# Kernel tuning notes

Hardware: AMD Instinct MI355X
Metric: run time of the kernel (lower is better)

## Reference

```python
import jax, jax.numpy as jnp
import numpy as np
import math

# Static config derived from init_kwargs
B, L, D, H, NL = 256, 256, 128, 2, 2
E = D // H                       # 64
F = L // 2 + 1                   # 129 rfft bins
SR = 0.6                         # sample_ratio (> 1/n_layers)
STEP = (F * (1.0 - SR)) // (NL - 1)          # 51.0, python float floor-div as in torch code
LEFTS = [int(F * (1.0 - SR) - k * STEP) for k in range(NL)]   # [51, 0]
RIGHTS = [int(F - k * STEP) for k in range(NL)]               # [129, 78]
TOPK = max(int(1 * math.log(L)), 1)          # factor=1 -> 5
NUM_TOTAL = 100000                           # user_num + item_num
SPATIAL_RATIO = 0.1
INV_SQRT_E = 1.0 / math.sqrt(E)
INV_SQRT_2 = 1.0 / math.sqrt(2.0)


def setup_inputs() -> dict:
    key = jax.random.key(0)
    ks = jax.random.split(key, 12)
    s = 0.05
    return {
        "paths": jax.random.randint(ks[0], (B, L), 0, NUM_TOTAL),
        "lengths": jax.random.randint(ks[1], (B,), 1, L + 1),
        "degrees": jax.random.randint(ks[2], (B,), 0, 64),
        "training": 1,
        "ego_emb": jax.random.normal(ks[3], (NUM_TOTAL + 1, D), jnp.float32) * s,
        "pos_emb": jax.random.normal(ks[4], (L, D), jnp.float32) * s,
        "Wq": jax.random.normal(ks[5], (NL, D, D), jnp.float32) * s,
        "Wk": jax.random.normal(ks[6], (NL, D, D), jnp.float32) * s,
        "Wv": jax.random.normal(ks[7], (NL, D, D), jnp.float32) * s,
        "Wp": jax.random.normal(ks[8], (NL, D, D), jnp.float32) * s,
        "F1": jax.random.normal(ks[9], (NL, D, 2 * D), jnp.float32) * s,
        "F2": jax.random.normal(ks[10], (NL, 2 * D, D), jnp.float32) * s,
    }


def _hybrid_attention(k, x, mask, Wq, Wk, Wv, Wp):
    # project and split heads: [B,H,E,L]
    def proj(W):
        return (x @ W).reshape(B, L, H, E).transpose(0, 2, 3, 1)
    q, kk, v = proj(Wq), proj(Wk), proj(Wv)
    qf = jnp.fft.rfft(q, axis=-1)   # [B,H,E,F] complex
    kf = jnp.fft.rfft(kk, axis=-1)
    vf = jnp.fft.rfft(v, axis=-1)
    l, r = LEFTS[k], RIGHTS[k]
    # frequency-band attention: band-limited cross-correlation (scatter back == zero-pad)
    res = qf[..., l:r] * jnp.conj(kf[..., l:r])
    box = jnp.zeros(qf.shape, dtype=res.dtype).at[..., l:r].set(res)
    corr = jnp.fft.irfft(box, n=L, axis=-1)          # [B,H,E,L]
    mean_value = jnp.mean(corr, axis=(1, 2))         # [B,L]
    # training branch: global topk delays (shared across batch), roll-based aggregation
    _, delays = jax.lax.top_k(jnp.mean(mean_value, axis=0), TOPK)   # [TOPK]
    weights = mean_value[:, delays]                  # [B,TOPK]
    tmp_corr = jax.nn.softmax(weights, axis=-1)      # [B,TOPK]
    # roll(v, -d) along time == gather at (t + d) % L
    idx = (jnp.arange(L)[None, :] + delays[:, None]) % L            # [TOPK,L]
    gathered = v[:, :, :, idx]                       # [B,H,E,TOPK,L]
    freq = jnp.einsum('bhetl,bt->bhel', gathered, tmp_corr)
    freq = freq.transpose(0, 3, 1, 2).reshape(B, L, D)
    # dual-domain: time attention on band-limited signals (std=True -> same band)
    def band_ifft(f):
        padded = jnp.zeros(f.shape, dtype=f.dtype).at[..., l:r].set(f[..., l:r])
        return jnp.fft.irfft(padded, n=L, axis=-1).transpose(0, 1, 3, 2)   # [B,H,L,E]
    qt, kt, vt = band_ifft(qf), band_ifft(kf), band_ifft(vf)
    scores = jnp.einsum('bhqe,bhke->bhqk', qt, kt) * INV_SQRT_E + mask
    att = jax.nn.softmax(scores, axis=-1)
    spatial = jnp.einsum('bhqk,bhke->bhqe', att, vt).transpose(0, 2, 1, 3).reshape(B, L, D)
    out = (1.0 - SPATIAL_RATIO) * freq + SPATIAL_RATIO * spatial
    return out @ Wp + x


def reference(paths, lengths, degrees, training, ego_emb, pos_emb, Wq, Wk, Wv, Wp, F1, F2):
    del degrees, training  # degrees unused; training branch baked in (training=True)
    x = ego_emb[paths] + pos_emb[None, :, :]         # [B,L,D]
    m = (paths < NUM_TOTAL).astype(jnp.float32)
    mask = ((1.0 - m) * -10000.0)[:, None, None, :]  # [B,1,1,L]
    for k in range(NL):
        a = _hybrid_attention(k, x, mask, Wq[k], Wk[k], Wv[k], Wp[k])
        h = a @ F1[k]
        h = h * 0.5 * (1.0 + jax.lax.erf(h * INV_SQRT_2))   # exact GELU
        x = h @ F2[k]
    # gather last valid position per sequence
    return x[jnp.arange(B), lengths - 1]             # [B,D]
```

## Files before the change

kernel.cpp:

```cpp
#include <hip/hip_runtime.h>
#include <math.h>

#define Bn 256
#define Ln 256
#define Dn 128
#define Hn 2
#define En 64
#define NLn 2
#define TOPKn 5
#define NUM_TOTALn 100000
#define BLD (Bn*Ln*Dn)
#define WT_LAYER 147456

using frag_ab = __attribute__((ext_vector_type(8))) short;
using frag_cd = __attribute__((ext_vector_type(4))) float;

__device__ inline short f2bf(float f) {
    union { float f; unsigned u; } c; c.f = f;
    unsigned r = (c.u + 0x7FFFu + ((c.u >> 16) & 1u)) >> 16;
    return (short)r;
}
__device__ inline float bf2f(short s) {
    union { unsigned u; float f; } c; c.u = ((unsigned)(unsigned short)s) << 16;
    return c.f;
}

__global__ void beacon_kernel(float* out, float v) { out[0] = v; }

__global__ __launch_bounds__(256) void build_G_kernel(short* __restrict__ G) {
    int k = blockIdx.x, t = blockIdx.y, s = threadIdx.x;
    int d = (t - s) & 255;
    int f1 = (k == 0) ? 51 : 1;
    int f2 = (k == 0) ? 127 : 77;
    float acc;
    if (d == 0) {
        acc = 2.0f * (float)(f2 - f1 + 1);
    } else {
        const float c = 3.14159265358979323846f / 256.0f;
        int ahi = (d * (2 * f2 + 1)) & 511;
        int alo = (d * (2 * f1 - 1)) & 511;
        acc = (sinf(c * (float)ahi) - sinf(c * (float)alo)) / sinf(c * (float)d);
    }
    acc += (k == 0) ? ((d & 1) ? -1.0f : 1.0f)
                    : 1.0f;
    G[((size_t)k * 256 + t) * 256 + s] = f2bf(acc * (1.0f / 256.0f));
}

__global__ __launch_bounds__(256) void build_x_kernel(const int* __restrict__ paths,
                                                      const float* __restrict__ ego,
                                                      const float* __restrict__ pos,
                                                      short* __restrict__ x) {
    int base = (blockIdx.x * 256 + threadIdx.x) * 4;
    int d = base & 127;
    int bl = base >> 7;
    int t = bl & 255;
    float4 e = *(const float4*)(ego + (size_t)paths[bl] * Dn + d);
    float4 p = *(const float4*)(pos + t * Dn + d);
    short4 s;
    s.x = f2bf(e.x + p.x); s.y = f2bf(e.y + p.y);
    s.z = f2bf(e.z + p.z); s.w = f2bf(e.w + p.w);
    *(short4*)&x[base] = s;
}

__global__ __launch_bounds__(256) void wtrans_all_kernel(
        const float* __restrict__ Wq, const float* __restrict__ Wk,
        const float* __restrict__ Wv, const float* __restrict__ Wp,
        const float* __restrict__ F1, const float* __restrict__ F2,
        short* __restrict__ Wt) {
    int z = blockIdx.y;
    int idx = blockIdx.x * 256 + threadIdx.x;
    short* WtL = Wt + (size_t)z * WT_LAYER;
    if (idx < 65536) {
        int which = idx >> 14, local = idx & 16383;
        const float* src = (which == 0) ? Wq : (which == 1) ? Wk
                         : (which == 2) ? Wv : Wp;
        float scale = (which == 3) ? 0.1f : 1.0f;
        int n = local & 127, k = local >> 7;
        WtL[(which << 14) + n * 128 + k] = f2bf(scale * src[(size_t)z * 16384 + local]);
    } else if (idx < 98304) {
        int local = idx - 65536;
        int n = local & 255, k = local >> 8;
        WtL[65536 + n * 128 + k] = f2bf(F1[(size_t)z * 32768 + local]);
    } else {
        int local = idx - 98304;
        int n = local & 127, k = local >> 7;
        WtL[98304 + n * 256 + k] = f2bf(F2[(size_t)z * 32768 + local]);
    }
}

template<bool BT_FAST, bool GELU_EPI>
__global__ __launch_bounds__(256)
void mfma_gemm_kernel(const short* A, const short* Bp, short* C, const short* R,
                      int K, int lda, int ldb, int ldc, int ldr,
                      long long sA, long long sB, long long sC, long long sR,
                      long long sCsplit, float alpha, float beta) {
    int bz = blockIdx.z;
    A += (size_t)bz * sA; C += (size_t)bz * sC;
    if (R) R += (size_t)bz * sR;
    const short* Bt = Bp + (size_t)bz * sB;
    const int m0 = blockIdx.x * 128, n0 = blockIdx.y * 128;
    int n0c = n0;
    if (sCsplit) { C += (size_t)blockIdx.y * sCsplit; n0c = 0; }
    __shared__ short As[128 * 40];
    __shared__ short Bs[128 * 40];
    int tid = threadIdx.x;
    int lane = tid & 63, wave = tid >> 6;
    int wr = (wave >> 1) * 64, wc = (wave & 1) * 64;
    int l15 = lane & 15, qd = lane >> 4;

    frag_cd zero4 = {0.f, 0.f, 0.f, 0.f};
    frag_cd acc[4][4];
    #pragma unroll
    for (int i = 0; i < 4; i++)
        #pragma unroll
        for (int j = 0; j < 4; j++) acc[i][j] = zero4;

    int arow = tid >> 1, acg = (tid & 1) * 16;
    int bnrow = tid >> 1, bcg = (tid & 1) * 16;
    int bkk = tid & 31, bnb = (tid >> 5) * 16;

    int4 pa0, pa1, pb0, pb1;
    {
        const short* ap = A + (size_t)(m0 + arow) * lda + acg;
        pa0 = *(const int4*)ap; pa1 = *(const int4*)(ap + 8);
        if (BT_FAST) {
            const short* bp = Bt + (size_t)(n0 + bnrow) * ldb + bcg;
            pb0 = *(const int4*)bp; pb1 = *(const int4*)(bp + 8);
        } else {
            const short* bp = Bt + (size_t)bkk * ldb + n0 + bnb;
            pb0 = *(const int4*)bp; pb1 = *(const int4*)(bp + 8);
        }
    }

    for (int k0 = 0; k0 < K; k0 += 32) {
        __syncthreads();
        *(int4*)&As[arow * 40 + acg] = pa0;
        *(int4*)&As[arow * 40 + acg + 8] = pa1;
        if (BT_FAST) {
            *(int4*)&Bs[bnrow * 40 + bcg] = pb0;
            *(int4*)&Bs[bnrow * 40 + bcg + 8] = pb1;
        } else {
            short tmp[16];
            *(int4*)&tmp[0] = pb0; *(int4*)&tmp[8] = pb1;
            #pragma unroll
            for (int i = 0; i < 16; i++) Bs[(bnb + i) * 40 + bkk] = tmp[i];
        }
        __syncthreads();
        if (k0 + 32 < K) {
            const short* ap = A + (size_t)(m0 + arow) * lda + k0 + 32 + acg;
            pa0 = *(const int4*)ap; pa1 = *(const int4*)(ap + 8);
            if (BT_FAST) {
                const short* bp = Bt + (size_t)(n0 + bnrow) * ldb + k0 + 32 + bcg;
                pb0 = *(const int4*)bp; pb1 = *(const int4*)(bp + 8);
            } else {
                const short* bp = Bt + (size_t)(k0 + 32 + bkk) * ldb + n0 + bnb;
                pb0 = *(const int4*)bp; pb1 = *(const int4*)(bp + 8);
            }
        }
        frag_ab af[4], bf[4];
        #pragma unroll
        for (int ms = 0; ms < 4; ms++)
            af[ms] = *(frag_ab*)&As[(wr + ms * 16 + l15) * 40 + qd * 8];
        #pragma unroll
        for (int ns = 0; ns < 4; ns++)
            bf[ns] = *(frag_ab*)&Bs[(wc + ns * 16 + l15) * 40 + qd * 8];
        #pragma unroll
        for (int ms = 0; ms < 4; ms++)
            #pragma unroll
            for (int ns = 0; ns < 4; ns++)
                acc[ms][ns] = __builtin_amdgcn_mfma_f32_16x16x32_bf16(
                    bf[ns], af[ms], acc[ms][ns], 0, 0, 0);
    }
    #pragma unroll
    for (int ms = 0; ms < 4; ms++) {
        int m = m0 + wr + ms * 16 + l15;
        #pragma unroll
        for (int ns = 0; ns < 4; ns++) {
            int nb = wc + ns * 16 + qd * 4;
            float v[4];
            #pragma unroll
            for (int r = 0; r < 4; r++) v[r] = alpha * acc[ms][ns][r];
            if (R) {
                short4 r4 = *(const short4*)&R[(size_t)m * ldr + n0 + nb];
                v[0] += beta * bf2f(r4.x); v[1] += beta * bf2f(r4.y);
                v[2] += beta * bf2f(r4.z); v[3] += beta * bf2f(r4.w);
            }
            if (GELU_EPI) {
                #pragma unroll
                for (int r = 0; r < 4; r++)
                    v[r] = v[r] * 0.5f * (1.0f + erff(v[r] * 0.70710678118654752f));
            }
            short4 o;
            o.x = f2bf(v[0]); o.y = f2bf(v[1]); o.z = f2bf(v[2]); o.w = f2bf(v[3]);
            *(short4*)&C[(size_t)m * ldc + n0c + nb] = o;
        }
    }
}

static inline void mgemm(hipStream_t s, const short* A, const short* B, short* C,
                         const short* R, int M, int N, int K,
                         int lda, int ldb, int ldc, int ldr,
                         long long sA, long long sB, long long sC, long long sR,
                         int batch, float alpha, float beta, bool btFast, bool gelu,
                         long long sCsplit = 0) {
    dim3 grid(M / 128, N / 128, batch), block(256);
    if (btFast) {
        if (gelu) mfma_gemm_kernel<true, true ><<<grid, block, 0, s>>>(A, B, C, R, K, lda, ldb, ldc, ldr, sA, sB, sC, sR, sCsplit, alpha, beta);
        else      mfma_gemm_kernel<true, false><<<grid, block, 0, s>>>(A, B, C, R, K, lda, ldb, ldc, ldr, sA, sB, sC, sR, sCsplit, alpha, beta);
    } else {
        if (gelu) mfma_gemm_kernel<false, true ><<<grid, block, 0, s>>>(A, B, C, R, K, lda, ldb, ldc, ldr, sA, sB, sC, sR, sCsplit, alpha, beta);
        else      mfma_gemm_kernel<false, false><<<grid, block, 0, s>>>(A, B, C, R, K, lda, ldb, ldc, ldr, sA, sB, sC, sR, sCsplit, alpha, beta);
    }
}

__global__ __launch_bounds__(512)
void filtproj_kernel(const short* __restrict__ G, const short* __restrict__ x,
                     const short* __restrict__ W, short* __restrict__ q) {
    int b = blockIdx.x;
    __shared__ short As[256 * 40];
    __shared__ short Bs[128 * 40];
    __shared__ short xf[256 * 136];
    int tid = threadIdx.x;
    int lane = tid & 63, wave = tid >> 6;
    int wr = (wave & 3) * 64, wc = (wave >> 2) * 64;
    int l15 = lane & 15, qd = lane >> 4;
    const short* xb = x + ((size_t)b << 15);

    frag_cd zero4 = {0.f, 0.f, 0.f, 0.f};
    frag_cd acc[4][4];
    #pragma unroll
    for (int i = 0; i < 4; i++)
        #pragma unroll
        for (int j = 0; j < 4; j++) acc[i][j] = zero4;

    int arow = tid >> 1, acg = (tid & 1) * 16;
    int bkk = tid & 31, bnb = (tid >> 5) * 16;

    int4 pa0, pa1, pb0, pb1;
    {
        const short* ap = G + (size_t)arow * 256 + acg;
        pa0 = *(const int4*)ap; pa1 = *(const int4*)(ap + 8);
        if (tid < 256) {
            const short* bp = xb + (size_t)bkk * 128 + bnb;
            pb0 = *(const int4*)bp; pb1 = *(const int4*)(bp + 8);
        }
    }
    for (int k0 = 0; k0 < 256; k0 += 32) {
        __syncthreads();
        *(int4*)&As[arow * 40 + acg] = pa0;
        *(int4*)&As[arow * 40 + acg + 8] = pa1;
        if (tid < 256) {
            short tmp[16];
            *(int4*)&tmp[0] = pb0; *(int4*)&tmp[8] = pb1;
            #pragma unroll
            for (int i = 0; i < 16; i++) Bs[(bnb + i) * 40 + bkk] = tmp[i];
        }
        __syncthreads();
        if (k0 + 32 < 256) {
            const short* ap = G + (size_t)arow * 256 + k0 + 32 + acg;
            pa0 = *(const int4*)ap; pa1 = *(const int4*)(ap + 8);
            if (tid < 256) {
                const short* bp = xb + (size_t)(k0 + 32 + bkk) * 128 + bnb;
                pb0 = *(const int4*)bp; pb1 = *(const int4*)(bp + 8);
            }
        }
        frag_ab af[4], bf[4];
        #pragma unroll
        for (int ms = 0; ms < 4; ms++)
            af[ms] = *(frag_ab*)&As[(wr + ms * 16 + l15) * 40 + qd * 8];
        #pragma unroll
        for (int ns = 0; ns < 4; ns++)
            bf[ns] = *(frag_ab*)&Bs[(wc + ns * 16 + l15) * 40 + qd * 8];
        #pragma unroll
        for (int ms = 0; ms < 4; ms++)
            #pragma unroll
            for (int ns = 0; ns < 4; ns++)
                acc[ms][ns] = __builtin_amdgcn_mfma_f32_16x16x32_bf16(
                    bf[ns], af[ms], acc[ms][ns], 0, 0, 0);
    }
    #pragma unroll
    for (int ms = 0; ms < 4; ms++) {
        int m = wr + ms * 16 + l15;
        #pragma unroll
        for (int ns = 0; ns < 4; ns++) {
            int nb = wc + ns * 16 + qd * 4;
            short4 o;
            o.x = f2bf(acc[ms][ns][0]); o.y = f2bf(acc[ms][ns][1]);
            o.z = f2bf(acc[ms][ns][2]); o.w = f2bf(acc[ms][ns][3]);
            *(short4*)&xf[m * 136 + nb] = o;
        }
    }

    int brow = tid >> 2, bcg = (tid & 3) * 8;
    #pragma unroll 1
    for (int y = 0; y < 3; y++) {
        const short* Bt = W + y * 16384;
        #pragma unroll
        for (int i = 0; i < 4; i++)
            #pragma unroll
            for (int j = 0; j < 4; j++) acc[i][j] = zero4;
        int4 pb = *(const int4*)(Bt + (size_t)brow * 128 + bcg);
        for (int k0 = 0; k0 < 128; k0 += 32) {
            __syncthreads();
            *(int4*)&Bs[brow * 40 + bcg] = pb;
            __syncthreads();
            if (k0 + 32 < 128)
                pb = *(const int4*)(Bt + (size_t)brow * 128 + k0 + 32 + bcg);
            frag_ab af[4], bf[4];
            #pragma unroll
            for (int ms = 0; ms < 4; ms++)
                af[ms] = *(frag_ab*)&xf[(wr + ms * 16 + l15) * 136 + k0 + qd * 8];
            #pragma unroll
            for (int ns = 0; ns < 4; ns++)
                bf[ns] = *(frag_ab*)&Bs[(wc + ns * 16 + l15) * 40 + qd * 8];
            #pragma unroll
            for (int ms = 0; ms < 4; ms++)
                #pragma unroll
                for (int ns = 0; ns < 4; ns++)
                    acc[ms][ns] = __builtin_amdgcn_mfma_f32_16x16x32_bf16(
                        bf[ns], af[ms], acc[ms][ns], 0, 0, 0);
        }
        short* Cy = q + (size_t)y * BLD + ((size_t)b << 15);
        #pragma unroll
        for (int ms = 0; ms < 4; ms++) {
            int m = wr + ms * 16 + l15;
            #pragma unroll
            for (int ns = 0; ns < 4; ns++) {
                int nb = wc + ns * 16 + qd * 4;
                short4 o;
                o.x = f2bf(acc[ms][ns][0]); o.y = f2bf(acc[ms][ns][1]);
                o.z = f2bf(acc[ms][ns][2]); o.w = f2bf(acc[ms][ns][3]);
                *(short4*)&Cy[(size_t)m * 128 + nb] = o;
            }
        }
    }
}

__global__ __launch_bounds__(512)
void amix_ffn_kernel(const short* __restrict__ x, const short* __restrict__ q,
                     const short* __restrict__ W,
                     const float* __restrict__ tc, const int* __restrict__ delays,
                     short* __restrict__ xout) {
    int b = blockIdx.x;
    __shared__ short aL[256 * 132];
    __shared__ short hA[256 * 132];
    int tid = threadIdx.x;
    int lane = tid & 63, wave = tid >> 6;
    int wr = (wave & 3) * 64, wc = (wave >> 2) * 64;
    int l15 = lane & 15, qd = lane >> 4;
    const short* xb = x + ((size_t)b << 15);

    float wj[TOPKn]; int dj[TOPKn];
    #pragma unroll
    for (int j = 0; j < TOPKn; j++) {
        wj[j] = tc[b * TOPKn + j];
        dj[j] = delays[j];
    }

    frag_cd zero4 = {0.f, 0.f, 0.f, 0.f};

    {
        int arow = tid >> 1, acg = (tid & 1) * 16;
        #pragma unroll
        for (int k0 = 0; k0 < 128; k0 += 32) {
            #pragma unroll
            for (int c = 0; c < 2; c++) {
                int col = k0 + acg + c * 8;
                float m8[8] = {0.f, 0.f, 0.f, 0.f, 0.f, 0.f, 0.f, 0.f};
                #pragma unroll
                for (int j = 0; j < TOPKn; j++) {
                    frag_ab v = *(const frag_ab*)(xb + (((arow + dj[j]) & 255) << 7) + col);
                    #pragma unroll
                    for (int i = 0; i < 8; i++) m8[i] += wj[j] * bf2f(v[i]);
                }
                frag_ab o;
                #pragma unroll
                for (int i = 0; i < 8; i++) o[i] = f2bf(m8[i]);
                *(frag_ab*)&hA[arow * 132 + col] = o;
            }
        }
        const short* qb = q + ((size_t)b << 15);
        #pragma unroll
        for (int p = 0; p < 8; p++) {
            int chunk = p * 512 + tid;
            int r = chunk >> 4, cb = (chunk & 15) * 8;
            *(frag_ab*)&aL[r * 132 + cb] = *(const frag_ab*)(qb + (size_t)r * 128 + cb);
        }
    }
    __syncthreads();

    frag_cd acc[4][4];
    #pragma unroll
    for (int i = 0; i < 4; i++)
        #pragma unroll
        for (int j = 0; j < 4; j++) acc[i][j] = zero4;
    {
        const short* Bt = W + 131072;
        for (int k0 = 0; k0 < 128; k0 += 32) {
            frag_ab af[4], bf[4];
            #pragma unroll
            for (int ms = 0; ms < 4; ms++)
                af[ms] = *(frag_ab*)&hA[(wr + ms * 16 + l15) * 132 + k0 + qd * 8];
            #pragma unroll
            for (int ns = 0; ns < 4; ns++)
                bf[ns] = *(const frag_ab*)(Bt + (size_t)(wc + ns * 16 + l15) * 128 + k0 + qd * 8);
            #pragma unroll
            for (int ms = 0; ms < 4; ms++)
                #pragma unroll
                for (int ns = 0; ns < 4; ns++)
                    acc[ms][ns] = __builtin_amdgcn_mfma_f32_16x16x32_bf16(
                        bf[ns], af[ms], acc[ms][ns], 0, 0, 0);
        }
    }
    {
        const short* Bt = W + 49152;
        for (int k0 = 0; k0 < 128; k0 += 32) {
            frag_ab af[4], bf[4];
            #pragma unroll
            for (int ms = 0; ms < 4; ms++)
                af[ms] = *(frag_ab*)&aL[(wr + ms * 16 + l15) * 132 + k0 + qd * 8];
            #pragma unroll
            for (int ns = 0; ns < 4; ns++)
                bf[ns] = *(const frag_ab*)(Bt + (size_t)(wc + ns * 16 + l15) * 128 + k0 + qd * 8);
            #pragma unroll
            for (int ms = 0; ms < 4; ms++)
                #pragma unroll
                for (int ns = 0; ns < 4; ns++)
                    acc[ms][ns] = __builtin_amdgcn_mfma_f32_16x16x32_bf16(
                        bf[ns], af[ms], acc[ms][ns], 0, 0, 0);
        }
    }
    __syncthreads();
    #pragma unroll
    for (int ms = 0; ms < 4; ms++) {
        int m = wr + ms * 16 + l15;
        #pragma unroll
        for (int ns = 0; ns < 4; ns++) {
            int nb = wc + ns * 16 + qd * 4;
            short4 r4 = *(const short4*)&xb[(size_t)m * 128 + nb];
            float v[4];
            v[0] = acc[ms][ns][0] + bf2f(r4.x);
            v[1] = acc[ms][ns][1] + bf2f(r4.y);
            v[2] = acc[ms][ns][2] + bf2f(r4.z);
            v[3] = acc[ms][ns][3] + bf2f(r4.w);
            short4 o;
            o.x = f2bf(v[0]); o.y = f2bf(v[1]); o.z = f2bf(v[2]); o.w = f2bf(v[3]);
            *(short4*)&aL[m * 132 + nb] = o;
        }
    }
    __syncthreads();

    const short* F1T = W + 65536;
    const short* F2T = W + 98304;
    frag_cd xacc[4][4];
    #pragma unroll
    for (int i = 0; i < 4; i++)
        #pragma unroll
        for (int j = 0; j < 4; j++) xacc[i][j] = zero4;

    #pragma unroll 1
    for (int half = 0; half < 2; half++) {
        const short* B1 = F1T + (size_t)(half * 128) * 128;
        frag_cd hacc[4][4];
        #pragma unroll
        for (int i = 0; i < 4; i++)
            #pragma unroll
            for (int j = 0; j < 4; j++) hacc[i][j] = zero4;
        for (int k0 = 0; k0 < 128; k0 += 32) {
            frag_ab af[4], bf[4];
            #pragma unroll
            for (int ms = 0; ms < 4; ms++)
                af[ms] = *(frag_ab*)&aL[(wr + ms * 16 + l15) * 132 + k0 + qd * 8];
            #pragma unroll
            for (int ns = 0; ns < 4; ns++)
                bf[ns] = *(const frag_ab*)(B1 + (size_t)(wc + ns * 16 + l15) * 128 + k0 + qd * 8);
            #pragma unroll
            for (int ms = 0; ms < 4; ms++)
                #pragma unroll
                for (int ns = 0; ns < 4; ns++)
                    hacc[ms][ns] = __builtin_amdgcn_mfma_f32_16x16x32_bf16(
                        bf[ns], af[ms], hacc[ms][ns], 0, 0, 0);
        }
        __syncthreads();
        #pragma unroll
        for (int ms = 0; ms < 4; ms++) {
            int m = wr + ms * 16 + l15;
            #pragma unroll
            for (int ns = 0; ns < 4; ns++) {
                int nb = wc + ns * 16 + qd * 4;
                float v[4];
                #pragma unroll
                for (int r = 0; r < 4; r++) {
                    float t = hacc[ms][ns][r];
                    v[r] = t * 0.5f * (1.0f + erff(t * 0.70710678118654752f));
                }
                short4 o;
                o.x = f2bf(v[0]); o.y = f2bf(v[1]);
                o.z = f2bf(v[2]); o.w = f2bf(v[3]);
                *(short4*)&hA[m * 132 + nb] = o;
            }
        }
        __syncthreads();

        for (int k0 = 0; k0 < 128; k0 += 32) {
            frag_ab af[4], bf[4];
            #pragma unroll
            for (int ms = 0; ms < 4; ms++)
                af[ms] = *(frag_ab*)&hA[(wr + ms * 16 + l15) * 132 + k0 + qd * 8];
            #pragma unroll
            for (int ns = 0; ns < 4; ns++)
                bf[ns] = *(const frag_ab*)(F2T + (size_t)(wc + ns * 16 + l15) * 256 + half * 128 + k0 + qd * 8);
            #pragma unroll
            for (int ms = 0; ms < 4; ms++)
                #pragma unroll
                for (int ns = 0; ns < 4; ns++)
                    xacc[ms][ns] = __builtin_amdgcn_mfma_f32_16x16x32_bf16(
                        bf[ns], af[ms], xacc[ms][ns], 0, 0, 0);
        }
    }
    short* xo = xout + ((size_t)b << 15);
    #pragma unroll
    for (int ms = 0; ms < 4; ms++) {
        int m = wr + ms * 16 + l15;
        #pragma unroll
        for (int ns = 0; ns < 4; ns++) {
            int nb = wc + ns * 16 + qd * 4;
            short4 o;
            o.x = f2bf(xacc[ms][ns][0]); o.y = f2bf(xacc[ms][ns][1]);
            o.z = f2bf(xacc[ms][ns][2]); o.w = f2bf(xacc[ms][ns][3]);
            *(short4*)&xo[(size_t)m * 128 + nb] = o;
        }
    }
}

__global__ __launch_bounds__(512, 4) void attn_kernel(short* q,
        const short* __restrict__ kb, const short* __restrict__ vf,
        const int* __restrict__ paths, float* __restrict__ mv2) {
    int h = blockIdx.x, b = blockIdx.y;
    __shared__ short SB[256 * 72];
    __shared__ short ks[64 * 72];
    __shared__ short vT[80 * 72];
    __shared__ float masks[256];
    __shared__ float mvpart[512];
    int tid = threadIdx.x;
    int lane = tid & 63, wave = tid >> 6;
    int l15 = lane & 15, qd = lane >> 4;
    if (tid < 256) masks[tid] = (paths[b * 256 + tid] < NUM_TOTALn) ? 0.0f : -10000.0f;
    {
        int e0 = tid * 2;
        #pragma unroll
        for (int i = 0; i < 2; i++) {
            int e = e0 + i;
            int row = 64 + (e >> 6), col = e & 63;
            vT[row * 72 + col] = (row == 64) ? (short)0x3F80 : (short)0;
        }
    }
    short* qg = q + ((size_t)b << 15) + (size_t)h * 64;
    const short* kg = kb + ((size_t)b << 15) + (size_t)h * 64;
    const short* vg = vf + ((size_t)b << 15) + (size_t)h * 64;

    #pragma unroll
    for (int p = 0; p < 4; p++) {
        int chunk = p * 512 + tid;
        int r = chunk >> 3, cb = (chunk & 7) * 8;
        *(frag_ab*)&SB[r * 72 + cb] = *(const frag_ab*)(qg + (size_t)r * 128 + cb);
    }
    __syncthreads();
    int myrow = wave * 32;
    frag_ab aq[2][2];
    #pragma unroll
    for (int mt = 0; mt < 2; mt++)
        #pragma unroll
        for (int hf = 0; hf < 2; hf++)
            aq[mt][hf] = *(frag_ab*)&SB[(myrow + mt * 16 + l15) * 72 + hf * 32 + qd * 8];

    frag_cd zero4 = {0.f, 0.f, 0.f, 0.f};
    frag_cd oacc[2][5];
    #pragma unroll
    for (int mt = 0; mt < 2; mt++)
        #pragma unroll
        for (int et = 0; et < 5; et++) oacc[mt][et] = zero4;
    float macc = 0.0f;
    int tau = tid & 255, half = tid >> 8;

    for (int jt = 0; jt < 4; jt++) {
        __syncthreads();
        {
            int r = tid >> 3, cb = (tid & 7) * 8;
            *(frag_ab*)&ks[r * 72 + cb] =
                *(const frag_ab*)(kg + (size_t)(jt * 64 + r) * 128 + cb);
            frag_ab v8 = *(const frag_ab*)(vg + (size_t)(jt * 64 + r) * 128 + cb);
            int swz = (((r >> 3) ^ (cb >> 3)) << 3) + (r & 7);
            #pragma unroll
            for (int i = 0; i < 8; i++) vT[(cb + i) * 72 + swz] = v8[i];
        }
        __syncthreads();
        #pragma unroll
        for (int mt = 0; mt < 2; mt++) {
            #pragma unroll
            for (int nt = 0; nt < 4; nt++) {
                frag_ab b0 = *(frag_ab*)&ks[(nt * 16 + l15) * 72 + qd * 8];
                frag_ab b1 = *(frag_ab*)&ks[(nt * 16 + l15) * 72 + 32 + qd * 8];
                frag_cd c = zero4;
                c = __builtin_amdgcn_mfma_f32_16x16x32_bf16(aq[mt][0], b0, c, 0, 0, 0);
                c = __builtin_amdgcn_mfma_f32_16x16x32_bf16(aq[mt][1], b1, c, 0, 0, 0);
                int keyLocal = nt * 16 + l15;
                #pragma unroll
                for (int r = 0; r < 4; r++) {
                    int row = myrow + mt * 16 + qd * 4 + r;
                    int tt = (row - jt * 64 - keyLocal) & 255;
                    SB[tt * 66 + keyLocal] = f2bf(c[r] * 0.125f);
                }
            }
        }
        __syncthreads();
        {
            const int* SD32 = (const int*)&SB[tau * 66 + half * 32];
            #pragma unroll
            for (int i = 0; i < 16; i++) {
                int pk = SD32[i];
                macc += bf2f((short)(pk & 0xFFFF)) + bf2f((short)(pk >> 16));
            }
        }
        #pragma unroll
        for (int mt = 0; mt < 2; mt++) {
            int row = myrow + mt * 16 + l15;
            #pragma unroll
            for (int hf = 0; hf < 2; hf++) {
                int kl0 = hf * 32 + qd * 8;
                frag_ab pfrag;
                #pragma unroll
                for (int j = 0; j < 8; j++) {
                    int kl = kl0 + j;
                    int tt = (row - jt * 64 - kl) & 255;
                    float s = bf2f(SB[tt * 66 + kl]);
                    pfrag[j] = f2bf(__expf(s + masks[jt * 64 + kl]));
                }
                #pragma unroll
                for (int et = 0; et < 5; et++) {
                    int e = et * 16 + l15;
                    int blk = (hf * 4 + qd) ^ ((e >> 3) & 7);
                    frag_ab bv = *(frag_ab*)&vT[e * 72 + (blk << 3)];
                    oacc[mt][et] = __builtin_amdgcn_mfma_f32_16x16x32_bf16(pfrag, bv, oacc[mt][et], 0, 0, 0);
                }
            }
        }
    }
    __syncthreads();
    mvpart[tid] = macc;
    __syncthreads();
    if (tid < 256)
        mv2[(size_t)h * 65536 + b * 256 + tid] =
            (mvpart[tid] + mvpart[tid + 256]) * 0.0625f;
    #pragma unroll
    for (int mt = 0; mt < 2; mt++) {
        #pragma unroll
        for (int r = 0; r < 4; r++) {
            float l = oacc[mt][4][r];
            l = __shfl(l, (lane & 48));
            float inv = 1.0f / l;
            int row = myrow + mt * 16 + qd * 4 + r;
            #pragma unroll
            for (int et = 0; et < 4; et++)
                qg[(size_t)row * 128 + et * 16 + l15] = f2bf(oacc[mt][et][r] * inv);
        }
    }
}

__global__ __launch_bounds__(256) void gm_reduce_kernel(const float* __restrict__ mv2,
                                                        float* __restrict__ gm) {
    int tau = blockIdx.x;
    int b = threadIdx.x;
    __shared__ float red[256];
    red[b] = mv2[b * 256 + tau] + mv2[65536 + b * 256 + tau];
    __syncthreads();
    for (int s = 128; s > 0; s >>= 1) { if (b < s) red[b] += red[b + s]; __syncthreads(); }
    if (b == 0) gm[tau] = red[0] * (1.0f / 256.0f);
}

__global__ __launch_bounds__(256) void topk_softmax_kernel(const float* __restrict__ gm,
                                                           const float* __restrict__ mv2,
                                                           int* __restrict__ delays,
                                                           float* __restrict__ tc) {
    __shared__ float vsh[4];
    __shared__ int ish[4];
    __shared__ int dsh[TOPKn];
    int tid = threadIdx.x;
    int lane = tid & 63, wave = tid >> 6;
    float v = gm[tid];
    for (int t = 0; t < TOPKn; t++) {
        float mv_ = v; int mi = tid;
        #pragma unroll
        for (int s = 32; s > 0; s >>= 1) {
            float v2 = __shfl_xor(mv_, s); int i2 = __shfl_xor(mi, s);
            if (v2 > mv_ || (v2 == mv_ && i2 < mi)) { mv_ = v2; mi = i2; }
        }
        if (lane == 0) { vsh[wave] = mv_; ish[wave] = mi; }
        __syncthreads();
        if (tid == 0) {
            float bv = vsh[0]; int bi = ish[0];
            #pragma unroll
            for (int w = 1; w < 4; w++)
                if (vsh[w] > bv || (vsh[w] == bv && ish[w] < bi)) { bv = vsh[w]; bi = ish[w]; }
            dsh[t] = bi; delays[t] = bi;
        }
        __syncthreads();
        if (tid == dsh[t]) v = -1e30f;
    }
    __syncthreads();
    int b = tid;
    float w[TOPKn];
    float m = -1e30f;
    #pragma unroll
    for (int j = 0; j < TOPKn; j++) {
        w[j] = mv2[b * 256 + dsh[j]] + mv2[65536 + b * 256 + dsh[j]];
        m = fmaxf(m, w[j]);
    }
    float ssum = 0.0f;
    #pragma unroll
    for (int j = 0; j < TOPKn; j++) { w[j] = expf(w[j] - m); ssum += w[j]; }
    #pragma unroll
    for (int j = 0; j < TOPKn; j++) tc[b * TOPKn + j] = w[j] / ssum;
}

__global__ __launch_bounds__(256) void gather_out_kernel(const short* __restrict__ x,
                                                         const int* __restrict__ lengths,
                                                         float* __restrict__ out) {
    int idx = blockIdx.x * 256 + threadIdx.x;
    int d = idx & 127;
    int b = idx >> 7;
    out[idx] = bf2f(x[((size_t)b << 15) + (size_t)(lengths[b] - 1) * Dn + d]);
}

extern "C" void kernel_launch(void* const* d_in, const int* in_sizes, int n_in,
                              void* d_out, int out_size, void* d_ws, size_t ws_size,
                              hipStream_t stream) {
    const int* paths    = (const int*)d_in[0];
    const int* lengths  = (const int*)d_in[1];
    const float* ego    = (const float*)d_in[4];
    const float* pos    = (const float*)d_in[5];
    const float* Wq     = (const float*)d_in[6];
    const float* Wk     = (const float*)d_in[7];
    const float* Wv     = (const float*)d_in[8];
    const float* Wp     = (const float*)d_in[9];
    const float* F1     = (const float*)d_in[10];
    const float* F2     = (const float*)d_in[11];
    float* out = (float*)d_out;

    const size_t need = (size_t)5 * BLD * 2 + 131072 * 2 + 131072 * 4
                        + 256 * 4 + 1280 * 4 + 16 * 4 + (size_t)NLn * WT_LAYER * 2;
    if (ws_size < need) {
        beacon_kernel<<<dim3(1), dim3(1), 0, stream>>>(out, (float)(ws_size >> 20));
        return;
    }

    short* x    = (short*)d_ws;
    short* q    = x + (size_t)1 * BLD;
    short* kb   = x + (size_t)2 * BLD;
    short* vf   = x + (size_t)3 * BLD;
    short* Gb   = x + (size_t)5 * BLD;
    float* mv   = (float*)(Gb + 131072);
    float* gm   = mv + 131072;
    float* tc   = gm + 256;
    int* delays = (int*)(tc + 1280);
    short* Wt   = (short*)(delays + 16);

    build_G_kernel<<<dim3(2, 256), dim3(256), 0, stream>>>(Gb);
    build_x_kernel<<<dim3(BLD / 1024), dim3(256), 0, stream>>>(paths, ego, pos, x);

    wtrans_all_kernel<<<dim3(512, NLn), dim3(256), 0, stream>>>(Wq, Wk, Wv, Wp, F1, F2, Wt);
    mgemm(stream, Wt + 49152, Wt + 32768, Wt + 131072, nullptr,
          128, 128, 128, 128, 128, 128, 0,
          WT_LAYER, WT_LAYER, WT_LAYER, 0, NLn,
          9.0f, 0.0f, false, false);

    for (int k = 0; k < NLn; k++) {
        const short* WtL = Wt + (size_t)k * WT_LAYER;
        filtproj_kernel<<<dim3(256), dim3(512), 0, stream>>>(
            Gb + (size_t)k * 65536, x, WtL, q);

        attn_kernel<<<dim3(2, 256), dim3(512), 0, stream>>>(q, kb, vf, paths, mv);

        gm_reduce_kernel<<<dim3(256), dim3(256), 0, stream>>>(mv, gm);
        topk_softmax_kernel<<<dim3(1), dim3(256), 0, stream>>>(gm, mv, delays, tc);

        amix_ffn_kernel<<<dim3(256), dim3(512), 0, stream>>>(
            x, q, WtL, tc, delays, x);
    }

    gather_out_kernel<<<dim3((Bn * Dn) / 256), dim3(256), 0, stream>>>(x, lengths, out);
}
```

Before: 364.5 us.

## Split amix_ffn across two row-half blocks and stage weight tiles in LDS

The fused auto-correlation mix plus FFN kernel now launches two 256-thread blocks per batch element, each handling 128 sequence rows. This halves per-block shared memory so more blocks can be resident and gives more blocks overall. Weight fragments for every GEMM stage are now staged through a small LDS tile with a register prefetch of the next k-slice, instead of being read straight from global memory by every wave. The kernel still updates x in place, but a block now reads delay-shifted rows that may belong to the other half while that half's block writes them, which is a cross-block read/write race.

New measurement: 357.9 us. Within noise of the previous version (-1.8%).

```diff
diff --git a/kernel.cpp b/kernel.cpp
--- a/kernel.cpp
+++ b/kernel.cpp
@@ -336,17 +336,19 @@
     }
 }
 
-__global__ __launch_bounds__(512)
+__global__ __launch_bounds__(256)
 void amix_ffn_kernel(const short* __restrict__ x, const short* __restrict__ q,
                      const short* __restrict__ W,
                      const float* __restrict__ tc, const int* __restrict__ delays,
                      short* __restrict__ xout) {
-    int b = blockIdx.x;
-    __shared__ short aL[256 * 132];
-    __shared__ short hA[256 * 132];
+    int half = blockIdx.x, b = blockIdx.y;
+    const int m0 = half * 128;
+    __shared__ short aL[128 * 132];
+    __shared__ short hA[128 * 132];
+    __shared__ short Bs[128 * 40];
     int tid = threadIdx.x;
     int lane = tid & 63, wave = tid >> 6;
-    int wr = (wave & 3) * 64, wc = (wave >> 2) * 64;
+    int wr = (wave >> 1) * 64, wc = (wave & 1) * 64;
     int l15 = lane & 15, qd = lane >> 4;
     const short* xb = x + ((size_t)b << 15);
 
@@ -369,7 +371,7 @@
                 float m8[8] = {0.f, 0.f, 0.f, 0.f, 0.f, 0.f, 0.f, 0.f};
                 #pragma unroll
                 for (int j = 0; j < TOPKn; j++) {
-                    frag_ab v = *(const frag_ab*)(xb + (((arow + dj[j]) & 255) << 7) + col);
+                    frag_ab v = *(const frag_ab*)(xb + (((m0 + arow + dj[j]) & 255) << 7) + col);
                     #pragma unroll
                     for (int i = 0; i < 8; i++) m8[i] += wj[j] * bf2f(v[i]);
                 }
@@ -379,31 +381,45 @@
                 *(frag_ab*)&hA[arow * 132 + col] = o;
             }
         }
-        const short* qb = q + ((size_t)b << 15);
+        const short* qb = q + ((size_t)b << 15) + (size_t)m0 * 128;
         #pragma unroll
         for (int p = 0; p < 8; p++) {
-            int chunk = p * 512 + tid;
+            int chunk = p * 256 + tid;
             int r = chunk >> 4, cb = (chunk & 15) * 8;
             *(frag_ab*)&aL[r * 132 + cb] = *(const frag_ab*)(qb + (size_t)r * 128 + cb);
         }
     }
     __syncthreads();
 
+    int brow = tid >> 1, bcg = (tid & 1) * 16;
+
     frag_cd acc[4][4];
     #pragma unroll
     for (int i = 0; i < 4; i++)
         #pragma unroll
         for (int j = 0; j < 4; j++) acc[i][j] = zero4;
-    {
-        const short* Bt = W + 131072;
+    #pragma unroll 1
+    for (int pass = 0; pass < 2; pass++) {
+        const short* Bt = W + (pass ? 49152 : 131072);
+        const short* Asrc = pass ? aL : hA;
+        int4 pb0 = *(const int4*)(Bt + (size_t)brow * 128 + bcg);
+        int4 pb1 = *(const int4*)(Bt + (size_t)brow * 128 + bcg + 8);
         for (int k0 = 0; k0 < 128; k0 += 32) {
+            __syncthreads();
+            *(int4*)&Bs[brow * 40 + bcg] = pb0;
+            *(int4*)&Bs[brow * 40 + bcg + 8] = pb1;
+            __syncthreads();
+            if (k0 + 32 < 128) {
+                pb0 = *(const int4*)(Bt + (size_t)brow * 128 + k0 + 32 + bcg);
+                pb1 = *(const int4*)(Bt + (size_t)brow * 128 + k0 + 32 + bcg + 8);
+            }
             frag_ab af[4], bf[4];
             #pragma unroll
             for (int ms = 0; ms < 4; ms++)
-                af[ms] = *(frag_ab*)&hA[(wr + ms * 16 + l15) * 132 + k0 + qd * 8];
+                af[ms] = *(frag_ab*)&Asrc[(wr + ms * 16 + l15) * 132 + k0 + qd * 8];
             #pragma unroll
             for (int ns = 0; ns < 4; ns++)
-                bf[ns] = *(const frag_ab*)(Bt + (size_t)(wc + ns * 16 + l15) * 128 + k0 + qd * 8);
+                bf[ns] = *(frag_ab*)&Bs[(wc + ns * 16 + l15) * 40 + qd * 8];
             #pragma unroll
             for (int ms = 0; ms < 4; ms++)
                 #pragma unroll
@@ -412,24 +428,6 @@
                         bf[ns], af[ms], acc[ms][ns], 0, 0, 0);
         }
     }
-    {
-        const short* Bt = W + 49152;
-        for (int k0 = 0; k0 < 128; k0 += 32) {
-            frag_ab af[4], bf[4];
-            #pragma unroll
-            for (int ms = 0; ms < 4; ms++)
-                af[ms] = *(frag_ab*)&aL[(wr + ms * 16 + l15) * 132 + k0 + qd * 8];
-            #pragma unroll
-            for (int ns = 0; ns < 4; ns++)
-                bf[ns] = *(const frag_ab*)(Bt + (size_t)(wc + ns * 16 + l15) * 128 + k0 + qd * 8);
-            #pragma unroll
-            for (int ms = 0; ms < 4; ms++)
-                #pragma unroll
-                for (int ns = 0; ns < 4; ns++)
-                    acc[ms][ns] = __builtin_amdgcn_mfma_f32_16x16x32_bf16(
-                        bf[ns], af[ms], acc[ms][ns], 0, 0, 0);
-        }
-    }
     __syncthreads();
     #pragma unroll
     for (int ms = 0; ms < 4; ms++) {
@@ -437,7 +435,7 @@
         #pragma unroll
         for (int ns = 0; ns < 4; ns++) {
             int nb = wc + ns * 16 + qd * 4;
-            short4 r4 = *(const short4*)&xb[(size_t)m * 128 + nb];
+            short4 r4 = *(const short4*)&xb[(size_t)(m0 + m) * 128 + nb];
             float v[4];
             v[0] = acc[ms][ns][0] + bf2f(r4.x);
             v[1] = acc[ms][ns][1] + bf2f(r4.y);
@@ -459,27 +457,39 @@
         for (int j = 0; j < 4; j++) xacc[i][j] = zero4;
 
     #pragma unroll 1
-    for (int half = 0; half < 2; half++) {
-        const short* B1 = F1T + (size_t)(half * 128) * 128;
+    for (int f1h = 0; f1h < 2; f1h++) {
+        const short* B1 = F1T + (size_t)(f1h * 128) * 128;
         frag_cd hacc[4][4];
         #pragma unroll
         for (int i = 0; i < 4; i++)
             #pragma unroll
             for (int j = 0; j < 4; j++) hacc[i][j] = zero4;
-        for (int k0 = 0; k0 < 128; k0 += 32) {
-            frag_ab af[4], bf[4];
-            #pragma unroll
-            for (int ms = 0; ms < 4; ms++)
-                af[ms] = *(frag_ab*)&aL[(wr + ms * 16 + l15) * 132 + k0 + qd * 8];
-            #pragma unroll
-            for (int ns = 0; ns < 4; ns++)
-                bf[ns] = *(const frag_ab*)(B1 + (size_t)(wc + ns * 16 + l15) * 128 + k0 + qd * 8);
-            #pragma unroll
-            for (int ms = 0; ms < 4; ms++)
+        {
+            int4 pb0 = *(const int4*)(B1 + (size_t)brow * 128 + bcg);
+            int4 pb1 = *(const int4*)(B1 + (size_t)brow * 128 + bcg + 8);
+            for (int k0 = 0; k0 < 128; k0 += 32) {
+                __syncthreads();
+                *(int4*)&Bs[brow * 40 + bcg] = pb0;
+                *(int4*)&Bs[brow * 40 + bcg + 8] = pb1;
+                __syncthreads();
+                if (k0 + 32 < 128) {
+                    pb0 = *(const int4*)(B1 + (size_t)brow * 128 + k0 + 32 + bcg);
+                    pb1 = *(const int4*)(B1 + (size_t)brow * 128 + k0 + 32 + bcg + 8);
+                }
+                frag_ab af[4], bf[4];
+                #pragma unroll
+                for (int ms = 0; ms < 4; ms++)
+                    af[ms] = *(frag_ab*)&aL[(wr + ms * 16 + l15) * 132 + k0 + qd * 8];
                 #pragma unroll
                 for (int ns = 0; ns < 4; ns++)
-                    hacc[ms][ns] = __builtin_amdgcn_mfma_f32_16x16x32_bf16(
-                        bf[ns], af[ms], hacc[ms][ns], 0, 0, 0);
+                    bf[ns] = *(frag_ab*)&Bs[(wc + ns * 16 + l15) * 40 + qd * 8];
+                #pragma unroll
+                for (int ms = 0; ms < 4; ms++)
+                    #pragma unroll
+                    for (int ns = 0; ns < 4; ns++)
+                        hacc[ms][ns] = __builtin_amdgcn_mfma_f32_16x16x32_bf16(
+                            bf[ns], af[ms], hacc[ms][ns], 0, 0, 0);
+            }
         }
         __syncthreads();
         #pragma unroll
@@ -502,23 +512,35 @@
         }
         __syncthreads();
 
-        for (int k0 = 0; k0 < 128; k0 += 32) {
-            frag_ab af[4], bf[4];
-            #pragma unroll
-            for (int ms = 0; ms < 4; ms++)
-                af[ms] = *(frag_ab*)&hA[(wr + ms * 16 + l15) * 132 + k0 + qd * 8];
-            #pragma unroll
-            for (int ns = 0; ns < 4; ns++)
-                bf[ns] = *(const frag_ab*)(F2T + (size_t)(wc + ns * 16 + l15) * 256 + half * 128 + k0 + qd * 8);
-            #pragma unroll
-            for (int ms = 0; ms < 4; ms++)
+        {
+            int4 pb0 = *(const int4*)(F2T + (size_t)brow * 256 + f1h * 128 + bcg);
+            int4 pb1 = *(const int4*)(F2T + (size_t)brow * 256 + f1h * 128 + bcg + 8);
+            for (int k0 = 0; k0 < 128; k0 += 32) {
+                __syncthreads();
+                *(int4*)&Bs[brow * 40 + bcg] = pb0;
+                *(int4*)&Bs[brow * 40 + bcg + 8] = pb1;
+                __syncthreads();
+                if (k0 + 32 < 128) {
+                    pb0 = *(const int4*)(F2T + (size_t)brow * 256 + f1h * 128 + k0 + 32 + bcg);
+                    pb1 = *(const int4*)(F2T + (size_t)brow * 256 + f1h * 128 + k0 + 32 + bcg + 8);
+                }
+                frag_ab af[4], bf[4];
+                #pragma unroll
+                for (int ms = 0; ms < 4; ms++)
+                    af[ms] = *(frag_ab*)&hA[(wr + ms * 16 + l15) * 132 + k0 + qd * 8];
                 #pragma unroll
                 for (int ns = 0; ns < 4; ns++)
-                    xacc[ms][ns] = __builtin_amdgcn_mfma_f32_16x16x32_bf16(
-                        bf[ns], af[ms], xacc[ms][ns], 0, 0, 0);
-        }
-    }
-    short* xo = xout + ((size_t)b << 15);
+                    bf[ns] = *(frag_ab*)&Bs[(wc + ns * 16 + l15) * 40 + qd * 8];
+                #pragma unroll
+                for (int ms = 0; ms < 4; ms++)
+                    #pragma unroll
+                    for (int ns = 0; ns < 4; ns++)
+                        xacc[ms][ns] = __builtin_amdgcn_mfma_f32_16x16x32_bf16(
+                            bf[ns], af[ms], xacc[ms][ns], 0, 0, 0);
+            }
+        }
+    }
+    short* xo = xout + ((size_t)b << 15) + (size_t)m0 * 128;
     #pragma unroll
     for (int ms = 0; ms < 4; ms++) {
         int m = wr + ms * 16 + l15;
@@ -784,7 +806,7 @@
         gm_reduce_kernel<<<dim3(256), dim3(256), 0, stream>>>(mv, gm);
         topk_softmax_kernel<<<dim3(1), dim3(256), 0, stream>>>(gm, mv, delays, tc);
 
-        amix_ffn_kernel<<<dim3(256), dim3(512), 0, stream>>>(
+        amix_ffn_kernel<<<dim3(2, 256), dim3(256), 0, stream>>>(
             x, q, WtL, tc, delays, x);
     }
 
```

## Stage weight tiles through double-buffered shared memory in amix_ffn GEMMs

Applied to the files above, without the earlier changes.

The B-operand (weight) fragments in all four GEMM loops of amix_ffn_kernel were read straight from global memory by every wave, with each weight row fetched by four waves. Now each 128x32 K-slice is loaded cooperatively, one int4 per thread, into a padded, double-buffered LDS tile, with the next slice prefetched into registers. This cuts duplicate global/L2 traffic and makes the loads coalesced. In exchange it adds a __syncthreads per K-step and about 20KB more LDS on top of about 135KB already used, which may be tight or limit occupancy.

Measured after the change: 352.0 us. 1.04x faster.

```diff
diff --git a/kernel.cpp b/kernel.cpp
--- a/kernel.cpp
+++ b/kernel.cpp
@@ -344,6 +344,7 @@
     int b = blockIdx.x;
     __shared__ short aL[256 * 132];
     __shared__ short hA[256 * 132];
+    __shared__ short Bs[2][128 * 40];
     int tid = threadIdx.x;
     int lane = tid & 63, wave = tid >> 6;
     int wr = (wave & 3) * 64, wc = (wave >> 2) * 64;
@@ -389,39 +390,31 @@
     }
     __syncthreads();
 
+    int brow = tid >> 2, bcg = (tid & 3) * 8;
+
     frag_cd acc[4][4];
     #pragma unroll
     for (int i = 0; i < 4; i++)
         #pragma unroll
         for (int j = 0; j < 4; j++) acc[i][j] = zero4;
-    {
-        const short* Bt = W + 131072;
-        for (int k0 = 0; k0 < 128; k0 += 32) {
+    #pragma unroll 1
+    for (int pass = 0; pass < 2; pass++) {
+        const short* Bt = W + (pass ? 49152 : 131072);
+        const short* Asrc = pass ? aL : hA;
+        int4 pb = *(const int4*)(Bt + (size_t)brow * 128 + bcg);
+        int cur = 0;
+        for (int k0 = 0; k0 < 128; k0 += 32, cur ^= 1) {
+            *(int4*)&Bs[cur][brow * 40 + bcg] = pb;
+            if (k0 + 32 < 128)
+                pb = *(const int4*)(Bt + (size_t)brow * 128 + k0 + 32 + bcg);
+            __syncthreads();
             frag_ab af[4], bf[4];
             #pragma unroll
             for (int ms = 0; ms < 4; ms++)
-                af[ms] = *(frag_ab*)&hA[(wr + ms * 16 + l15) * 132 + k0 + qd * 8];
+                af[ms] = *(frag_ab*)&Asrc[(wr + ms * 16 + l15) * 132 + k0 + qd * 8];
             #pragma unroll
             for (int ns = 0; ns < 4; ns++)
-                bf[ns] = *(const frag_ab*)(Bt + (size_t)(wc + ns * 16 + l15) * 128 + k0 + qd * 8);
-            #pragma unroll
-            for (int ms = 0; ms < 4; ms++)
-                #pragma unroll
-                for (int ns = 0; ns < 4; ns++)
-                    acc[ms][ns] = __builtin_amdgcn_mfma_f32_16x16x32_bf16(
-                        bf[ns], af[ms], acc[ms][ns], 0, 0, 0);
-        }
-    }
-    {
-        const short* Bt = W + 49152;
-        for (int k0 = 0; k0 < 128; k0 += 32) {
-            frag_ab af[4], bf[4];
-            #pragma unroll
-            for (int ms = 0; ms < 4; ms++)
-                af[ms] = *(frag_ab*)&aL[(wr + ms * 16 + l15) * 132 + k0 + qd * 8];
-            #pragma unroll
-            for (int ns = 0; ns < 4; ns++)
-                bf[ns] = *(const frag_ab*)(Bt + (size_t)(wc + ns * 16 + l15) * 128 + k0 + qd * 8);
+                bf[ns] = *(frag_ab*)&Bs[cur][(wc + ns * 16 + l15) * 40 + qd * 8];
             #pragma unroll
             for (int ms = 0; ms < 4; ms++)
                 #pragma unroll
@@ -466,20 +459,28 @@
         for (int i = 0; i < 4; i++)
             #pragma unroll
             for (int j = 0; j < 4; j++) hacc[i][j] = zero4;
-        for (int k0 = 0; k0 < 128; k0 += 32) {
-            frag_ab af[4], bf[4];
-            #pragma unroll
-            for (int ms = 0; ms < 4; ms++)
-                af[ms] = *(frag_ab*)&aL[(wr + ms * 16 + l15) * 132 + k0 + qd * 8];
-            #pragma unroll
-            for (int ns = 0; ns < 4; ns++)
-                bf[ns] = *(const frag_ab*)(B1 + (size_t)(wc + ns * 16 + l15) * 128 + k0 + qd * 8);
-            #pragma unroll
-            for (int ms = 0; ms < 4; ms++)
+        {
+            int4 pb = *(const int4*)(B1 + (size_t)brow * 128 + bcg);
+            int cur = 0;
+            for (int k0 = 0; k0 < 128; k0 += 32, cur ^= 1) {
+                *(int4*)&Bs[cur][brow * 40 + bcg] = pb;
+                if (k0 + 32 < 128)
+                    pb = *(const int4*)(B1 + (size_t)brow * 128 + k0 + 32 + bcg);
+                __syncthreads();
+                frag_ab af[4], bf[4];
+                #pragma unroll
+                for (int ms = 0; ms < 4; ms++)
+                    af[ms] = *(frag_ab*)&aL[(wr + ms * 16 + l15) * 132 + k0 + qd * 8];
                 #pragma unroll
                 for (int ns = 0; ns < 4; ns++)
-                    hacc[ms][ns] = __builtin_amdgcn_mfma_f32_16x16x32_bf16(
-                        bf[ns], af[ms], hacc[ms][ns], 0, 0, 0);
+                    bf[ns] = *(frag_ab*)&Bs[cur][(wc + ns * 16 + l15) * 40 + qd * 8];
+                #pragma unroll
+                for (int ms = 0; ms < 4; ms++)
+                    #pragma unroll
+                    for (int ns = 0; ns < 4; ns++)
+                        hacc[ms][ns] = __builtin_amdgcn_mfma_f32_16x16x32_bf16(
+                            bf[ns], af[ms], hacc[ms][ns], 0, 0, 0);
+            }
         }
         __syncthreads();
         #pragma unroll
@@ -502,20 +503,28 @@
         }
         __syncthreads();
 
-        for (int k0 = 0; k0 < 128; k0 += 32) {
-            frag_ab af[4], bf[4];
-            #pragma unroll
-            for (int ms = 0; ms < 4; ms++)
-                af[ms] = *(frag_ab*)&hA[(wr + ms * 16 + l15) * 132 + k0 + qd * 8];
-            #pragma unroll
-            for (int ns = 0; ns < 4; ns++)
-                bf[ns] = *(const frag_ab*)(F2T + (size_t)(wc + ns * 16 + l15) * 256 + half * 128 + k0 + qd * 8);
-            #pragma unroll
-            for (int ms = 0; ms < 4; ms++)
+        {
+            int4 pb = *(const int4*)(F2T + (size_t)brow * 256 + half * 128 + bcg);
+            int cur = 0;
+            for (int k0 = 0; k0 < 128; k0 += 32, cur ^= 1) {
+                *(int4*)&Bs[cur][brow * 40 + bcg] = pb;
+                if (k0 + 32 < 128)
+                    pb = *(const int4*)(F2T + (size_t)brow * 256 + half * 128 + k0 + 32 + bcg);
+                __syncthreads();
+                frag_ab af[4], bf[4];
+                #pragma unroll
+                for (int ms = 0; ms < 4; ms++)
+                    af[ms] = *(frag_ab*)&hA[(wr + ms * 16 + l15) * 132 + k0 + qd * 8];
                 #pragma unroll
                 for (int ns = 0; ns < 4; ns++)
-                    xacc[ms][ns] = __builtin_amdgcn_mfma_f32_16x16x32_bf16(
-                        bf[ns], af[ms], xacc[ms][ns], 0, 0, 0);
+                    bf[ns] = *(frag_ab*)&Bs[cur][(wc + ns * 16 + l15) * 40 + qd * 8];
+                #pragma unroll
+                for (int ms = 0; ms < 4; ms++)
+                    #pragma unroll
+                    for (int ns = 0; ns < 4; ns++)
+                        xacc[ms][ns] = __builtin_amdgcn_mfma_f32_16x16x32_bf16(
+                            bf[ns], af[ms], xacc[ms][ns], 0, 0, 0);
+            }
         }
     }
     short* xo = xout + ((size_t)b << 15);
```
